# Kernel optimization log

Measured on AMD Instinct MI355X. Metric: run time of the kernel, lower is better.

## Reference

```python
import jax, jax.numpy as jnp
import numpy as np


def setup_inputs() -> dict:
    key = jax.random.key(0)
    ks = jax.random.split(key, 4)
    B, IN, H, D, N = 512, 1024, 1024, 64, 512
    s = 0.02  # weight scale to keep gates in a sane range
    return {
        "x": jax.random.normal(ks[0], (B, IN), jnp.float32),
        "h0": jnp.zeros((B, H), jnp.float32),
        "c0": jnp.zeros((B, H), jnp.float32),
        "W_ih": jax.random.normal(ks[1], (4 * H, IN), jnp.float32) * s,
        "W_hh": jax.random.normal(ks[2], (4 * H, H), jnp.float32) * s,
        "b_ih": jnp.zeros((4 * H,), jnp.float32),
        "b_hh": jnp.zeros((4 * H,), jnp.float32),
        "W_out": jax.random.normal(ks[3], (N, H), jnp.float32) * s,
        "b_out": jnp.zeros((N,), jnp.float32),
        "D": D,
    }


def reference(x, h0, c0, W_ih, W_hh, b_ih, b_hh, W_out, b_out, D):
    # x is fed identically at every step -> precompute its gate contribution once.
    xW = x @ W_ih.T + b_ih  # (B, 4H)

    def step(carry, _):
        h, c = carry
        gates = xW + h @ W_hh.T + b_hh  # (B, 4H), torch gate order i,f,g,o
        i, f, g, o = jnp.split(gates, 4, axis=-1)
        c = jax.nn.sigmoid(f) * c + jax.nn.sigmoid(i) * jnp.tanh(g)
        h = jax.nn.sigmoid(o) * jnp.tanh(c)
        return (h, c), h @ W_out.T + b_out  # per-step action values (B, N)

    (_, _), outs = jax.lax.scan(step, (h0, c0), xs=None, length=D)
    return outs  # (D, B, N)
```

## Files before the change

### kernel.cpp

```cpp
#include <hip/hip_runtime.h>
#include <hip/hip_bf16.h>

#define BATCH 512
#define HDIM  1024
#define G4    4096
#define DSTEP 64
#define NOUT  512
#define HB    ((size_t)BATCH * HDIM)

typedef __bf16 bf16;
typedef __bf16 bf16x8 __attribute__((ext_vector_type(8)));
typedef float  f32x4  __attribute__((ext_vector_type(4)));

#define MFMA16(a, b, c) __builtin_amdgcn_mfma_f32_16x16x32_bf16((a), (b), (c), 0, 0, 0)

#define GLOAD_LDS16(g, l)                                                           \
    __builtin_amdgcn_global_load_lds((const __attribute__((address_space(1))) void*)(g), \
                                     (__attribute__((address_space(3))) void*)(l), 16, 0, 0)

__device__ __forceinline__ float sigmoid_f(float x) { return 1.0f / (1.0f + __expf(-x)); }
__device__ __forceinline__ float tanh_f(float x)    { return 1.0f - 2.0f / (__expf(2.0f * x) + 1.0f); }

__device__ __forceinline__ int swz4(int row) { return (row ^ (row >> 2)) & 3; }

__global__ void prep_kernel(const float* __restrict__ x, const float* __restrict__ h0,
                            const float* __restrict__ c0,
                            const float* __restrict__ W_ih, const float* __restrict__ W_hh,
                            const float* __restrict__ W_out,
                            bf16* __restrict__ x_b, bf16* __restrict__ Wih_b,
                            bf16* __restrict__ Whh_i, bf16* __restrict__ Wout_b,
                            bf16* __restrict__ h_slot0, float* __restrict__ c) {
    int tid = blockIdx.x * blockDim.x + threadIdx.x;
    int stride = gridDim.x * blockDim.x;
    for (int i = tid; i < G4 * HDIM; i += stride) {
        int r = i >> 10, k = i & 1023;
        int r2 = ((r & 1023) << 2) | (r >> 10);
        Whh_i[(size_t)r2 * HDIM + k] = (bf16)W_hh[i];
        Wih_b[i] = (bf16)W_ih[i];
    }
    for (int i = tid; i < BATCH * HDIM; i += stride) {
        x_b[i]     = (bf16)x[i];
        Wout_b[i]  = (bf16)W_out[i];
        h_slot0[i] = (bf16)h0[i];
        c[i]       = c0[i];
    }
}

template <int M, int N, int K, bool INTER>
__global__ __launch_bounds__(256) void gemm_bt_tiled(const bf16* __restrict__ A,
                                                     const bf16* __restrict__ Bw,
                                                     const float* __restrict__ bias,
                                                     const float* __restrict__ bias2,
                                                     float* __restrict__ C) {
    constexpr int MT = M / 128;
    constexpr int NT = N / 128;
    constexpr int TOT = MT * NT;
    __shared__ bf16 sA[2][128 * 32];
    __shared__ bf16 sB[2][128 * 32];

    int bid = blockIdx.x;
    int g = (bid & 7) * (TOT / 8) + (bid >> 3);
    int nt = g % NT, mt = g / NT;
    int mrow0 = mt * 128, ncol0 = nt * 128;

    int tid = threadIdx.x;
    int l = tid & 63;
    int w = tid >> 6;
    int wr = w >> 1, wc = w & 1;
    int lr = l & 15, q = l >> 4;

    const bf16* Abase = A + (size_t)mrow0 * K;
    const bf16* Bbase = Bw + (size_t)ncol0 * K;

    auto stage = [&](const bf16* base, bf16* dst, int k0) {
#pragma unroll
        for (int j = 0; j < 2; ++j) {
            int pbase = w * 64 + 256 * j;
            int p = pbase + l;
            int row = p >> 2, seg = p & 3;
            int sseg = seg ^ swz4(row);
            const bf16* gp = base + (size_t)row * K + k0 + sseg * 8;
            GLOAD_LDS16(gp, dst + pbase * 8);
        }
    };

    stage(Abase, sA[0], 0);
    stage(Bbase, sB[0], 0);
    __syncthreads();

    f32x4 acc[4][4] = {};
    constexpr int NS = K / 32;
    for (int s = 0; s < NS; ++s) {
        int cur = s & 1;
        if (s + 1 < NS) {
            stage(Abase, sA[cur ^ 1], (s + 1) * 32);
            stage(Bbase, sB[cur ^ 1], (s + 1) * 32);
        }
        bf16x8 af[4], bf[4];
#pragma unroll
        for (int fm = 0; fm < 4; ++fm) {
            int row = wr * 64 + fm * 16 + lr;
            af[fm] = *(const bf16x8*)&sA[cur][row * 32 + 8 * (q ^ swz4(row))];
        }
#pragma unroll
        for (int fn = 0; fn < 4; ++fn) {
            int row = wc * 64 + fn * 16 + lr;
            bf[fn] = *(const bf16x8*)&sB[cur][row * 32 + 8 * (q ^ swz4(row))];
        }
#pragma unroll
        for (int fm = 0; fm < 4; ++fm)
#pragma unroll
            for (int fn = 0; fn < 4; ++fn)
                acc[fm][fn] = MFMA16(af[fm], bf[fn], acc[fm][fn]);
        __syncthreads();
    }

#pragma unroll
    for (int fm = 0; fm < 4; ++fm)
#pragma unroll
        for (int fn = 0; fn < 4; ++fn) {
            int col = ncol0 + wc * 64 + fn * 16 + lr;
            float bs = bias[col] + (bias2 ? bias2[col] : 0.0f);
            int colw = INTER ? (((col & 1023) << 2) | (col >> 10)) : col;
#pragma unroll
            for (int r = 0; r < 4; ++r) {
                int row = mrow0 + wr * 64 + fm * 16 + q * 4 + r;
                C[(size_t)row * N + colw] = acc[fm][fn][r] + bs;
            }
        }
}

__global__ __launch_bounds__(512, 2) void lstm_step3(
    const bf16* __restrict__ h_prev,
    const bf16* __restrict__ Whh_i,
    const float* __restrict__ xWi,
    float* __restrict__ c,
    bf16* __restrict__ h_out)
{
    __shared__ __align__(16) char smem[131072];
    bf16*  A_lds = (bf16*)smem;
    float* red   = (float*)smem;
    float* gbuf  = (float*)(smem + 98304);

    int b  = blockIdx.x;
    int nb = ((b & 7) << 2) | ((b >> 3) & 3);
    int mb = b >> 5;

    int tid = threadIdx.x;
    int l   = tid & 63;
    int wid = tid >> 6;
    int kw  = wid >> 1;
    int cw  = wid & 1;
    int lr = l & 15, q = l >> 4;

    int row0 = mb * 64;

    const bf16* hsrc = h_prev + (size_t)row0 * HDIM;
#pragma unroll
    for (int jj = 0; jj < 16; ++jj) {
        int base = jj * 512 + wid * 64;
        int p = base + l;
        int rown = p >> 7, ss = p & 127;
        int sg = ss ^ (rown & 7);
        GLOAD_LDS16(hsrc + (size_t)rown * HDIM + sg * 8, A_lds + (size_t)base * 8);
    }
    __syncthreads();

    const bf16* Bbase = Whh_i + (size_t)(nb * 128 + cw * 64 + lr) * HDIM + kw * 256 + q * 8;
    f32x4 acc[4][4] = {};
#pragma unroll
    for (int kc = 0; kc < 8; ++kc) {
        bf16x8 bfr[4];
#pragma unroll
        for (int fn = 0; fn < 4; ++fn)
            bfr[fn] = *(const bf16x8*)(Bbase + (size_t)fn * 16 * HDIM + kc * 32);
        bf16x8 afr[4];
#pragma unroll
        for (int fm = 0; fm < 4; ++fm) {
            int rown = fm * 16 + lr;
            int s = kw * 32 + kc * 4 + q;
            afr[fm] = *(const bf16x8*)&A_lds[(size_t)(rown * 128 + (s ^ (rown & 7))) * 8];
        }
#pragma unroll
        for (int fm = 0; fm < 4; ++fm)
#pragma unroll
            for (int fn = 0; fn < 4; ++fn)
                acc[fm][fn] = MFMA16(afr[fm], bfr[fn], acc[fm][fn]);
    }
    __syncthreads();

    if (kw > 0) {
        float* dst = red + (size_t)((kw - 1) * 2 + cw) * 4096;
#pragma unroll
        for (int fm = 0; fm < 4; ++fm)
#pragma unroll
            for (int fn = 0; fn < 4; ++fn)
#pragma unroll
                for (int r = 0; r < 4; ++r)
                    dst[((fm * 4 + fn) * 4 + r) * 64 + l] = acc[fm][fn][r];
    }
    __syncthreads();
    if (kw == 0) {
#pragma unroll
        for (int fm = 0; fm < 4; ++fm)
#pragma unroll
            for (int fn = 0; fn < 4; ++fn) {
                int col = cw * 64 + fn * 16 + lr;
#pragma unroll
                for (int r = 0; r < 4; ++r) {
                    float v = acc[fm][fn][r];
#pragma unroll
                    for (int j = 0; j < 3; ++j)
                        v += red[(size_t)(j * 2 + cw) * 4096 + ((fm * 4 + fn) * 4 + r) * 64 + l];
                    int row = fm * 16 + q * 4 + r;
                    gbuf[row * 128 + (col ^ ((row & 7) << 2))] = v;
                }
            }
    }
    __syncthreads();

#pragma unroll
    for (int it = 0; it < 4; ++it) {
        int idx = it * 512 + tid;
        int row = idx >> 5, hl = idx & 31;
        int grow = row0 + row;
        int hcol = nb * 32 + hl;
        float4 g4 = *(const float4*)&gbuf[row * 128 + ((hl * 4) ^ ((row & 7) << 2))];
        float4 xw = *(const float4*)&xWi[(size_t)grow * G4 + (size_t)hcol * 4];
        float gi = g4.x + xw.x;
        float gf = g4.y + xw.y;
        float gg = g4.z + xw.z;
        float go = g4.w + xw.w;
        size_t cix = (size_t)grow * HDIM + hcol;
        float cn = sigmoid_f(gf) * c[cix] + sigmoid_f(gi) * tanh_f(gg);
        float hn = sigmoid_f(go) * tanh_f(cn);
        c[cix] = cn;
        h_out[cix] = (bf16)hn;
    }
}

extern "C" void kernel_launch(void* const* d_in, const int* in_sizes, int n_in,
                              void* d_out, int out_size, void* d_ws, size_t ws_size,
                              hipStream_t stream) {
    const float* x    = (const float*)d_in[0];
    const float* h0   = (const float*)d_in[1];
    const float* c0   = (const float*)d_in[2];
    const float* W_ih = (const float*)d_in[3];
    const float* W_hh = (const float*)d_in[4];
    const float* b_ih = (const float*)d_in[5];
    const float* b_hh = (const float*)d_in[6];
    const float* W_out= (const float*)d_in[7];
    const float* b_out= (const float*)d_in[8];

    char* ws = (char*)d_ws;
    bf16*  Whh_i  = (bf16*)(ws + 0);
    bf16*  Wih_b  = (bf16*)(ws + (size_t)(8 << 20));
    bf16*  x_b    = (bf16*)(ws + (size_t)(16 << 20));
    bf16*  Wout_b = (bf16*)(ws + (size_t)(17 << 20));
    float* xWbuf  = (float*)(ws + (size_t)(18 << 20));
    float* cbuf   = (float*)(ws + (size_t)(26 << 20));
    bf16*  h_all  = (bf16*)(ws + (size_t)(28 << 20));

    prep_kernel<<<2048, 256, 0, stream>>>(x, h0, c0, W_ih, W_hh, W_out,
                                          x_b, Wih_b, Whh_i, Wout_b, h_all, cbuf);

    gemm_bt_tiled<BATCH, G4, HDIM, true><<<128, 256, 0, stream>>>(x_b, Wih_b, b_ih, b_hh, xWbuf);

    for (int t = 0; t < DSTEP; ++t) {
        lstm_step3<<<256, 512, 0, stream>>>(h_all + (size_t)t * HB, Whh_i, xWbuf,
                                            cbuf, h_all + (size_t)(t + 1) * HB);
    }

    gemm_bt_tiled<DSTEP * BATCH, NOUT, HDIM, false><<<1024, 256, 0, stream>>>(
        h_all + HB, Wout_b, b_out, nullptr, (float*)d_out);
}
```

Measured before the change: 1.220 ms.

## Replace per-step LSTM launches with a persistent cooperative kernel using flag sync

The 64 per-timestep kernel launches become one cooperative persistent kernel. Each block keeps its W_hh slice in registers, keeps xW and the cell state in registers for all steps, and synchronises with the other blocks sharing its batch rows through a per-row-group atomic arrival counter. This removes launch overhead and the repeated W_hh and c reloads each step. In exchange it relies on relaxed atomics for visibility of h and on all 256 blocks being co-resident, and the large register footprint may cause spills.

```diff
diff --git a/kernel.cpp b/kernel.cpp
--- a/kernel.cpp
+++ b/kernel.cpp
@@ -1,5 +1,8 @@
 #include <hip/hip_runtime.h>
 #include <hip/hip_bf16.h>
+#include <hip/hip_cooperative_groups.h>
+
+namespace cg = cooperative_groups;
 
 #define BATCH 512
 #define HDIM  1024
@@ -11,6 +14,7 @@
 typedef __bf16 bf16;
 typedef __bf16 bf16x8 __attribute__((ext_vector_type(8)));
 typedef float  f32x4  __attribute__((ext_vector_type(4)));
+typedef unsigned long long u64;
 
 #define MFMA16(a, b, c) __builtin_amdgcn_mfma_f32_16x16x32_bf16((a), (b), (c), 0, 0, 0)
 
@@ -24,14 +28,14 @@
 __device__ __forceinline__ int swz4(int row) { return (row ^ (row >> 2)) & 3; }
 
 __global__ void prep_kernel(const float* __restrict__ x, const float* __restrict__ h0,
-                            const float* __restrict__ c0,
                             const float* __restrict__ W_ih, const float* __restrict__ W_hh,
                             const float* __restrict__ W_out,
                             bf16* __restrict__ x_b, bf16* __restrict__ Wih_b,
                             bf16* __restrict__ Whh_i, bf16* __restrict__ Wout_b,
-                            bf16* __restrict__ h_slot0, float* __restrict__ c) {
+                            bf16* __restrict__ h_slot0, unsigned int* __restrict__ flags) {
     int tid = blockIdx.x * blockDim.x + threadIdx.x;
     int stride = gridDim.x * blockDim.x;
+    if (blockIdx.x == 0 && threadIdx.x < 8) flags[threadIdx.x * 64] = 0;
     for (int i = tid; i < G4 * HDIM; i += stride) {
         int r = i >> 10, k = i & 1023;
         int r2 = ((r & 1023) << 2) | (r >> 10);
@@ -42,7 +46,6 @@
         x_b[i]     = (bf16)x[i];
         Wout_b[i]  = (bf16)W_out[i];
         h_slot0[i] = (bf16)h0[i];
-        c[i]       = c0[i];
     }
 }
 
@@ -130,21 +133,22 @@
         }
 }
 
-__global__ __launch_bounds__(512, 2) void lstm_step3(
-    const bf16* __restrict__ h_prev,
-    const bf16* __restrict__ Whh_i,
-    const float* __restrict__ xWi,
-    float* __restrict__ c,
-    bf16* __restrict__ h_out)
+__global__ __launch_bounds__(512) __attribute__((amdgpu_waves_per_eu(2, 2)))
+void persistent_lstm3(const bf16* __restrict__ Whh_i,
+                      const float* __restrict__ xWi,
+                      const float* __restrict__ c0,
+                      bf16* __restrict__ h_all,
+                      unsigned int* __restrict__ flags)
 {
     __shared__ __align__(16) char smem[131072];
     bf16*  A_lds = (bf16*)smem;
     float* red   = (float*)smem;
     float* gbuf  = (float*)(smem + 98304);
 
-    int b  = blockIdx.x;
-    int nb = ((b & 7) << 2) | ((b >> 3) & 3);
-    int mb = b >> 5;
+    int bid = blockIdx.x;
+    int mb = bid & 7;
+    int nb = bid >> 3;
+    unsigned int* arrive = flags + mb * 64;
 
     int tid = threadIdx.x;
     int l   = tid & 63;
@@ -154,88 +158,124 @@
     int lr = l & 15, q = l >> 4;
 
     int row0 = mb * 64;
-
-    const bf16* hsrc = h_prev + (size_t)row0 * HDIM;
-#pragma unroll
-    for (int jj = 0; jj < 16; ++jj) {
-        int base = jj * 512 + wid * 64;
-        int p = base + l;
-        int rown = p >> 7, ss = p & 127;
-        int sg = ss ^ (rown & 7);
-        GLOAD_LDS16(hsrc + (size_t)rown * HDIM + sg * 8, A_lds + (size_t)base * 8);
-    }
-    __syncthreads();
-
-    const bf16* Bbase = Whh_i + (size_t)(nb * 128 + cw * 64 + lr) * HDIM + kw * 256 + q * 8;
-    f32x4 acc[4][4] = {};
-#pragma unroll
-    for (int kc = 0; kc < 8; ++kc) {
-        bf16x8 bfr[4];
+    int gc0  = nb * 128 + cw * 64;
+
+    bf16x8 Breg[8][4];
+#pragma unroll
+    for (int kc = 0; kc < 8; ++kc)
 #pragma unroll
         for (int fn = 0; fn < 4; ++fn)
-            bfr[fn] = *(const bf16x8*)(Bbase + (size_t)fn * 16 * HDIM + kc * 32);
-        bf16x8 afr[4];
-#pragma unroll
-        for (int fm = 0; fm < 4; ++fm) {
-            int rown = fm * 16 + lr;
-            int s = kw * 32 + kc * 4 + q;
-            afr[fm] = *(const bf16x8*)&A_lds[(size_t)(rown * 128 + (s ^ (rown & 7))) * 8];
-        }
-#pragma unroll
-        for (int fm = 0; fm < 4; ++fm)
-#pragma unroll
-            for (int fn = 0; fn < 4; ++fn)
-                acc[fm][fn] = MFMA16(afr[fm], bfr[fn], acc[fm][fn]);
-    }
-    __syncthreads();
-
-    if (kw > 0) {
-        float* dst = red + (size_t)((kw - 1) * 2 + cw) * 4096;
-#pragma unroll
-        for (int fm = 0; fm < 4; ++fm)
-#pragma unroll
-            for (int fn = 0; fn < 4; ++fn)
-#pragma unroll
-                for (int r = 0; r < 4; ++r)
-                    dst[((fm * 4 + fn) * 4 + r) * 64 + l] = acc[fm][fn][r];
-    }
-    __syncthreads();
-    if (kw == 0) {
-#pragma unroll
-        for (int fm = 0; fm < 4; ++fm)
-#pragma unroll
-            for (int fn = 0; fn < 4; ++fn) {
-                int col = cw * 64 + fn * 16 + lr;
-#pragma unroll
-                for (int r = 0; r < 4; ++r) {
-                    float v = acc[fm][fn][r];
-#pragma unroll
-                    for (int j = 0; j < 3; ++j)
-                        v += red[(size_t)(j * 2 + cw) * 4096 + ((fm * 4 + fn) * 4 + r) * 64 + l];
-                    int row = fm * 16 + q * 4 + r;
-                    gbuf[row * 128 + (col ^ ((row & 7) << 2))] = v;
+            Breg[kc][fn] = *(const bf16x8*)&Whh_i[(size_t)(gc0 + fn * 16 + lr) * HDIM +
+                                                  kw * 256 + kc * 32 + q * 8];
+
+    int erow = tid >> 3, ecq = tid & 7;
+    int hcol0 = nb * 32 + ecq * 4;
+    int grow = row0 + erow;
+
+    float4 xws[4];
+#pragma unroll
+    for (int j = 0; j < 4; ++j)
+        xws[j] = *(const float4*)&xWi[(size_t)grow * G4 + (size_t)(hcol0 + j) * 4];
+    float4 cst = *(const float4*)&c0[(size_t)grow * HDIM + hcol0];
+    float cstv[4] = {cst.x, cst.y, cst.z, cst.w};
+
+    int srow = tid & 63, sgrp = tid >> 6;
+
+    for (int t = 0; t < DSTEP; ++t) {
+        const u64* gsrc = (const u64*)(h_all + (size_t)t * HB + (size_t)(row0 + srow) * HDIM +
+                                       sgrp * 128);
+        u64 lov[16], hiv[16];
+#pragma unroll
+        for (int k = 0; k < 16; ++k) {
+            lov[k] = __hip_atomic_load(gsrc + 2 * k,     __ATOMIC_RELAXED, __HIP_MEMORY_SCOPE_AGENT);
+            hiv[k] = __hip_atomic_load(gsrc + 2 * k + 1, __ATOMIC_RELAXED, __HIP_MEMORY_SCOPE_AGENT);
+        }
+#pragma unroll
+        for (int k = 0; k < 16; ++k) {
+            int sg = sgrp * 16 + k;
+            uint4 v;
+            v.x = (unsigned int)lov[k]; v.y = (unsigned int)(lov[k] >> 32);
+            v.z = (unsigned int)hiv[k]; v.w = (unsigned int)(hiv[k] >> 32);
+            *(uint4*)&A_lds[(size_t)(srow * 128 + (sg ^ (srow & 7))) * 8] = v;
+        }
+        __syncthreads();
+
+        f32x4 acc[4][4] = {};
+#pragma unroll
+        for (int kc = 0; kc < 8; ++kc) {
+            bf16x8 afr[4];
+#pragma unroll
+            for (int fm = 0; fm < 4; ++fm) {
+                int rown = fm * 16 + lr;
+                int s = kw * 32 + kc * 4 + q;
+                afr[fm] = *(const bf16x8*)&A_lds[(size_t)(rown * 128 + (s ^ (rown & 7))) * 8];
+            }
+#pragma unroll
+            for (int fm = 0; fm < 4; ++fm)
+#pragma unroll
+                for (int fn = 0; fn < 4; ++fn)
+                    acc[fm][fn] = MFMA16(afr[fm], Breg[kc][fn], acc[fm][fn]);
+        }
+        __syncthreads();
+
+        if (kw > 0) {
+            float* dst = red + (size_t)((kw - 1) * 2 + cw) * 4096;
+#pragma unroll
+            for (int fm = 0; fm < 4; ++fm)
+#pragma unroll
+                for (int fn = 0; fn < 4; ++fn)
+#pragma unroll
+                    for (int r = 0; r < 4; ++r)
+                        dst[((fm * 4 + fn) * 4 + r) * 64 + l] = acc[fm][fn][r];
+        }
+        __syncthreads();
+        if (kw == 0) {
+#pragma unroll
+            for (int fm = 0; fm < 4; ++fm)
+#pragma unroll
+                for (int fn = 0; fn < 4; ++fn) {
+                    int col = cw * 64 + fn * 16 + lr;
+#pragma unroll
+                    for (int r = 0; r < 4; ++r) {
+                        float v = acc[fm][fn][r];
+#pragma unroll
+                        for (int j = 0; j < 3; ++j)
+                            v += red[(size_t)(j * 2 + cw) * 4096 + ((fm * 4 + fn) * 4 + r) * 64 + l];
+                        int rowg = fm * 16 + q * 4 + r;
+                        gbuf[rowg * 128 + (col ^ ((rowg & 7) << 2))] = v;
+                    }
                 }
+        }
+        __syncthreads();
+
+        u64 pack = 0;
+#pragma unroll
+        for (int j = 0; j < 4; ++j) {
+            float4 g4 = *(const float4*)&gbuf[erow * 128 + ((ecq * 16 + j * 4) ^ ((erow & 7) << 2))];
+            float gi = g4.x + xws[j].x;
+            float gf = g4.y + xws[j].y;
+            float gg = g4.z + xws[j].z;
+            float go = g4.w + xws[j].w;
+            float cn = sigmoid_f(gf) * cstv[j] + sigmoid_f(gi) * tanh_f(gg);
+            float hn = sigmoid_f(go) * tanh_f(cn);
+            cstv[j] = cn;
+            bf16 hb = (bf16)hn;
+            unsigned short hu = *(unsigned short*)&hb;
+            pack |= (u64)hu << (16 * j);
+        }
+        __hip_atomic_store((u64*)(h_all + (size_t)(t + 1) * HB + (size_t)grow * HDIM + hcol0),
+                           pack, __ATOMIC_RELAXED, __HIP_MEMORY_SCOPE_AGENT);
+
+        if (t + 1 < DSTEP) {
+            __syncthreads();
+            if (tid == 0) {
+                __hip_atomic_fetch_add(arrive, 1u, __ATOMIC_RELAXED, __HIP_MEMORY_SCOPE_AGENT);
+                unsigned int target = 32u * (unsigned int)(t + 1);
+                while (__hip_atomic_load(arrive, __ATOMIC_RELAXED, __HIP_MEMORY_SCOPE_AGENT) < target)
+                    __builtin_amdgcn_s_sleep(2);
             }
-    }
-    __syncthreads();
-
-#pragma unroll
-    for (int it = 0; it < 4; ++it) {
-        int idx = it * 512 + tid;
-        int row = idx >> 5, hl = idx & 31;
-        int grow = row0 + row;
-        int hcol = nb * 32 + hl;
-        float4 g4 = *(const float4*)&gbuf[row * 128 + ((hl * 4) ^ ((row & 7) << 2))];
-        float4 xw = *(const float4*)&xWi[(size_t)grow * G4 + (size_t)hcol * 4];
-        float gi = g4.x + xw.x;
-        float gf = g4.y + xw.y;
-        float gg = g4.z + xw.z;
-        float go = g4.w + xw.w;
-        size_t cix = (size_t)grow * HDIM + hcol;
-        float cn = sigmoid_f(gf) * c[cix] + sigmoid_f(gi) * tanh_f(gg);
-        float hn = sigmoid_f(go) * tanh_f(cn);
-        c[cix] = cn;
-        h_out[cix] = (bf16)hn;
+            __syncthreads();
+        }
     }
 }
 
@@ -258,17 +298,24 @@
     bf16*  x_b    = (bf16*)(ws + (size_t)(16 << 20));
     bf16*  Wout_b = (bf16*)(ws + (size_t)(17 << 20));
     float* xWbuf  = (float*)(ws + (size_t)(18 << 20));
-    float* cbuf   = (float*)(ws + (size_t)(26 << 20));
+    unsigned int* flags = (unsigned int*)(ws + (size_t)(26 << 20));
     bf16*  h_all  = (bf16*)(ws + (size_t)(28 << 20));
 
-    prep_kernel<<<2048, 256, 0, stream>>>(x, h0, c0, W_ih, W_hh, W_out,
-                                          x_b, Wih_b, Whh_i, Wout_b, h_all, cbuf);
+    prep_kernel<<<2048, 256, 0, stream>>>(x, h0, W_ih, W_hh, W_out,
+                                          x_b, Wih_b, Whh_i, Wout_b, h_all, flags);
 
     gemm_bt_tiled<BATCH, G4, HDIM, true><<<128, 256, 0, stream>>>(x_b, Wih_b, b_ih, b_hh, xWbuf);
 
-    for (int t = 0; t < DSTEP; ++t) {
-        lstm_step3<<<256, 512, 0, stream>>>(h_all + (size_t)t * HB, Whh_i, xWbuf,
-                                            cbuf, h_all + (size_t)(t + 1) * HB);
+    {
+        const bf16*   whh_arg  = Whh_i;
+        const float*  xwi_arg  = xWbuf;
+        const float*  c0_arg   = c0;
+        bf16*         hall_arg = h_all;
+        unsigned int* flg_arg  = flags;
+        void* kargs[] = {(void*)&whh_arg, (void*)&xwi_arg, (void*)&c0_arg,
+                         (void*)&hall_arg, (void*)&flg_arg};
+        hipLaunchCooperativeKernel((const void*)persistent_lstm3, dim3(256), dim3(512),
+                                   kargs, 0, stream);
     }
 
     gemm_bt_tiled<DSTEP * BATCH, NOUT, HDIM, false><<<1024, 256, 0, stream>>>(
```

Result: slower. 2.296 ms (+88.2%).
